# Performance work log

Measured on AMD Instinct MI355X. Metric: run time of the kernel, lower is better.

The kernel has to match this reference:

```python
import jax, jax.numpy as jnp
import numpy as np

N_NODES = 50000
N_EDGES = 600000
IN_FEATS = 128
H_FEATS = 128
NUM_CLASSES = 64


def setup_inputs() -> dict:
    key = jax.random.key(0)
    k = jax.random.split(key, 8)
    x = jax.random.normal(k[0], (N_NODES, IN_FEATS), dtype=jnp.float32)
    W1 = jax.random.normal(k[1], (IN_FEATS, H_FEATS), dtype=jnp.float32) * (1.0 / np.sqrt(IN_FEATS))
    b1 = jnp.zeros((H_FEATS,), dtype=jnp.float32)
    W2 = jax.random.normal(k[2], (H_FEATS, NUM_CLASSES), dtype=jnp.float32) * (1.0 / np.sqrt(H_FEATS))
    b2 = jnp.zeros((NUM_CLASSES,), dtype=jnp.float32)
    src = jax.random.randint(k[3], (N_EDGES,), 0, N_NODES, dtype=jnp.int64)
    dst = jax.random.randint(k[4], (N_EDGES,), 0, N_NODES, dtype=jnp.int64)
    return {"x": x, "W1": W1, "b1": b1, "W2": W2, "b2": b2, "src": src, "dst": dst}


def _graph_conv(h, W, b, src, dst, norm_src, norm_dst, n_nodes):
    # DGL GraphConv, norm='both': scale by 1/sqrt(out_deg(src)), sum over edges,
    # scale by 1/sqrt(in_deg(dst)), then linear transform.
    h = h * norm_src[:, None]                                   # [N, F]
    m = jax.ops.segment_sum(h[src], dst, num_segments=n_nodes)  # [N, F] scatter-add over edges
    m = m * norm_dst[:, None]
    return m @ W + b


def reference(x, W1, b1, W2, b2, src, dst):
    n = x.shape[0]
    ones = jnp.ones(src.shape[0], dtype=x.dtype)
    deg_out = jax.ops.segment_sum(ones, src, num_segments=n)
    deg_in = jax.ops.segment_sum(ones, dst, num_segments=n)
    norm_src = jax.lax.rsqrt(jnp.maximum(deg_out, 1.0))
    norm_dst = jax.lax.rsqrt(jnp.maximum(deg_in, 1.0))
    h = _graph_conv(x, W1, b1, src, dst, norm_src, norm_dst, n)
    h = jax.nn.relu(h)
    out = _graph_conv(h, W2, b2, src, dst, norm_src, norm_dst, n)
    return out
```

## Files before the change

### kernel.cpp

```cpp
#include <hip/hip_runtime.h>
#include <hip/hip_fp16.h>

#define NN 50000
#define NE 600000
#define KF 128
#define OC1 128
#define OC2 64

#define HBLK 64
#define HCH ((NE + HBLK - 1) / HBLK)
#define HP4 (NN / 4)
#define NSCB 49
#define NGB ((NN + 63) / 64)

typedef _Float16 half8 __attribute__((ext_vector_type(8)));
typedef float floatx4 __attribute__((ext_vector_type(4)));

__launch_bounds__(256)
__global__ void wt_hist_kernel(const float* __restrict__ W1, const float* __restrict__ W2,
                               __half* __restrict__ Wt1, __half* __restrict__ Wt2,
                               const int* __restrict__ src, const int* __restrict__ dst,
                               int* __restrict__ Hs, int* __restrict__ Hd) {
    __shared__ int bins[HP4];
    if (blockIdx.x < 96) {
        int i = blockIdx.x * 256 + threadIdx.x;
        if (i < KF * OC1) {
            int k = i >> 7, c = i & (OC1 - 1);
            Wt1[c * KF + k] = __float2half(W1[i]);
        } else {
            int j = i - KF * OC1;
            int k = j >> 6, c = j & (OC2 - 1);
            Wt2[c * KF + k] = __float2half(W2[j]);
        }
        return;
    }
    const int b = blockIdx.x - 96;
    const bool is_src = (b < HBLK);
    const int bb = is_src ? b : b - HBLK;
    const int* key = is_src ? src : dst;
    int* H = is_src ? Hs : Hd;
    const int e0 = bb * HCH;
    const int e1 = min(e0 + HCH, NE);

    for (int i = threadIdx.x; i < HP4; i += 256) bins[i] = 0;
    __syncthreads();
    for (int e = e0 + threadIdx.x; e < e1; e += 256) {
        int v = key[e];
        atomicAdd(&bins[v >> 2], 1 << ((v & 3) * 8));
    }
    __syncthreads();
    int* o = H + (size_t)bb * HP4;
    for (int i = threadIdx.x; i < HP4; i += 256) o[i] = bins[i];
}

__launch_bounds__(256)
__global__ void rednorm_kernel(const int* __restrict__ Hs, const int* __restrict__ Hd,
                               int* __restrict__ deg_i, float* __restrict__ nsrc,
                               float* __restrict__ ndst, int* __restrict__ bsum) {
    __shared__ int red[256];
    const int tid = threadIdx.x;
    const int p = blockIdx.x * 256 + tid;
    int so0 = 0, so1 = 0, so2 = 0, so3 = 0, si0 = 0, si1 = 0, si2 = 0, si3 = 0;
    if (p < HP4) {
#pragma unroll 4
        for (int b = 0; b < HBLK; b++) {
            int hs = Hs[(size_t)b * HP4 + p];
            int hd = Hd[(size_t)b * HP4 + p];
            so0 += hs & 255; so1 += (hs >> 8) & 255; so2 += (hs >> 16) & 255; so3 += (hs >> 24) & 255;
            si0 += hd & 255; si1 += (hd >> 8) & 255; si2 += (hd >> 16) & 255; si3 += (hd >> 24) & 255;
        }
        reinterpret_cast<int4*>(deg_i)[p] = make_int4(si0, si1, si2, si3);
        reinterpret_cast<float4*>(nsrc)[p] =
            make_float4(rsqrtf(fmaxf((float)so0, 1.f)), rsqrtf(fmaxf((float)so1, 1.f)),
                        rsqrtf(fmaxf((float)so2, 1.f)), rsqrtf(fmaxf((float)so3, 1.f)));
        reinterpret_cast<float4*>(ndst)[p] =
            make_float4(rsqrtf(fmaxf((float)si0, 1.f)), rsqrtf(fmaxf((float)si1, 1.f)),
                        rsqrtf(fmaxf((float)si2, 1.f)), rsqrtf(fmaxf((float)si3, 1.f)));
    }
    red[tid] = si0 + si1 + si2 + si3;
    __syncthreads();
    for (int off = 128; off > 0; off >>= 1) {
        if (tid < off) red[tid] += red[tid + off];
        __syncthreads();
    }
    if (tid == 0) bsum[blockIdx.x] = red[0];
}

__launch_bounds__(256)
__global__ void scan_bofs_gemm1_kernel(const int* __restrict__ deg, const int* __restrict__ bsum,
                                       const int* __restrict__ Hd, int* __restrict__ ptr,
                                       unsigned int* __restrict__ Bofs,
                                       const float* __restrict__ x, const __half* __restrict__ Wt1,
                                       const float* __restrict__ nsrc, __half* __restrict__ g) {
    extern __shared__ char smem[];
    if (blockIdx.x < NSCB) {
        int* s = (int*)smem;
        int* sboff = (int*)(smem + 1024);
        const int tid = threadIdx.x;
        if (tid < 64) {
            int v = (tid < (int)blockIdx.x) ? bsum[tid] : 0;
#pragma unroll
            for (int off = 32; off > 0; off >>= 1) v += __shfl_xor(v, off);
            if (tid == 0) *sboff = v;
        }
        const int q = blockIdx.x * 256 + tid;
        int4 d = make_int4(0, 0, 0, 0);
        if (q < HP4) d = reinterpret_cast<const int4*>(deg)[q];
        int t4 = d.x + d.y + d.z + d.w;
        s[tid] = t4;
        __syncthreads();
        for (int off = 1; off < 256; off <<= 1) {
            int t = (tid >= off) ? s[tid - off] : 0;
            __syncthreads();
            s[tid] += t;
            __syncthreads();
        }
        if (q < HP4) {
            int base = *sboff + s[tid] - t4;
            int4 pv;
            pv.x = base;
            pv.y = base + d.x;
            pv.z = pv.y + d.y;
            pv.w = pv.z + d.z;
            reinterpret_cast<int4*>(ptr)[q] = pv;
        }
        if (blockIdx.x == 0 && tid == 0) ptr[NN] = NE;
        return;
    }
    if (blockIdx.x < 2 * NSCB) {
        int p = (blockIdx.x - NSCB) * 256 + threadIdx.x;
        if (p >= HP4) return;
        int r0 = 0, r1 = 0, r2 = 0, r3 = 0;
#pragma unroll 4
        for (int b = 0; b < HBLK; b++) {
            Bofs[(size_t)b * HP4 + p] =
                (unsigned)(r0 | (r1 << 8) | (r2 << 16) | (r3 << 24));
            int h = Hd[(size_t)b * HP4 + p];
            r0 += h & 255; r1 += (h >> 8) & 255; r2 += (h >> 16) & 255; r3 += (h >> 24) & 255;
        }
        return;
    }
    constexpr int NT = OC1 / 16;
    constexpr int LDK = KF + 8;
    _Float16* Wsh = (_Float16*)smem;

    const int tid = threadIdx.x;
    const int wave = tid >> 6;
    const int lane = tid & 63;
    const int l16 = lane & 15;
    const int koff = (lane >> 4) * 8;
    const int row0 = (blockIdx.x - 2 * NSCB) * 64;
    const int arow = row0 + wave * 16 + l16;

    for (int i = tid; i < OC1 * (KF / 8); i += 256) {
        int r = i >> 4;
        int c8 = i & 15;
        *reinterpret_cast<uint4*>(&Wsh[r * LDK + c8 * 8]) =
            reinterpret_cast<const uint4*>(Wt1 + (size_t)r * KF)[c8];
    }

    half8 afr[4];
    if (arow < NN) {
        const float* ap = x + (size_t)arow * KF + koff;
#pragma unroll
        for (int kk = 0; kk < 4; kk++) {
            float4 v0 = *reinterpret_cast<const float4*>(ap + kk * 32);
            float4 v1 = *reinterpret_cast<const float4*>(ap + kk * 32 + 4);
            half8 h;
            h[0] = (_Float16)v0.x; h[1] = (_Float16)v0.y;
            h[2] = (_Float16)v0.z; h[3] = (_Float16)v0.w;
            h[4] = (_Float16)v1.x; h[5] = (_Float16)v1.y;
            h[6] = (_Float16)v1.z; h[7] = (_Float16)v1.w;
            afr[kk] = h;
        }
    } else {
#pragma unroll
        for (int kk = 0; kk < 4; kk++) afr[kk] = (half8)(_Float16)0;
    }

    __syncthreads();

    floatx4 acc[NT];
#pragma unroll
    for (int n = 0; n < NT; n++) acc[n] = (floatx4)(0.f);

#pragma unroll
    for (int n = 0; n < NT; n++) {
        const int brow = n * 16 + l16;
#pragma unroll
        for (int kk = 0; kk < 4; kk++) {
            half8 bfr = *reinterpret_cast<const half8*>(&Wsh[brow * LDK + kk * 32 + koff]);
            acc[n] = __builtin_amdgcn_mfma_f32_16x16x32_f16(afr[kk], bfr, acc[n], 0, 0, 0);
        }
    }

    const int crow = row0 + wave * 16 + (lane >> 4) * 4;
    float nsv[4];
#pragma unroll
    for (int j = 0; j < 4; j++) {
        int rr = crow + j;
        nsv[j] = (rr < NN) ? nsrc[rr] : 0.f;
    }
#pragma unroll
    for (int n = 0; n < NT; n++) {
#pragma unroll
        for (int j = 0; j < 4; j++) {
            int rr = crow + j;
            if (rr < NN)
                g[(size_t)rr * OC1 + n * 16 + l16] = __float2half(acc[n][j] * nsv[j]);
        }
    }
}

__launch_bounds__(256)
__global__ void fill_kernel(const int* __restrict__ src, const int* __restrict__ dst,
                            const unsigned int* __restrict__ Bofs,
                            const int* __restrict__ ptr, int* __restrict__ esrc) {
    __shared__ int cnt[HP4];
    const int b = blockIdx.x;
    const int e0 = b * HCH;
    const int e1 = min(e0 + HCH, NE);
    for (int i = threadIdx.x; i < HP4; i += 256) cnt[i] = 0;
    __syncthreads();
    const unsigned char* B = (const unsigned char*)(Bofs + (size_t)b * HP4);
    for (int e = e0 + threadIdx.x; e < e1; e += 256) {
        int v = dst[e];
        int sh = (v & 3) * 8;
        int old = atomicAdd(&cnt[v >> 2], 1 << sh);
        int idx = (old >> sh) & 255;
        esrc[ptr[v] + (int)B[v] + idx] = src[e];
    }
}

__launch_bounds__(256)
__global__ void gathergemm2_kernel(const __half* __restrict__ g, const int* __restrict__ ptr,
                                   const int* __restrict__ esrc, const float* __restrict__ ndst,
                                   const float* __restrict__ nsrc, const float* __restrict__ b1,
                                   const __half* __restrict__ Wt2, __half* __restrict__ g2) {
    constexpr int LDK = KF + 8;
    __shared__ _Float16 h1sh[64 * LDK];
    __shared__ _Float16 Wsh[OC2 * LDK];

    const int tid = threadIdx.x;
    const int node0 = blockIdx.x * 64;

    for (int i = tid; i < OC2 * (KF / 8); i += 256) {
        int r = i >> 4;
        int c8 = i & 15;
        *reinterpret_cast<uint4*>(&Wsh[r * LDK + c8 * 8]) =
            reinterpret_cast<const uint4*>(Wt2 + (size_t)r * KF)[c8];
    }

    const int qw = tid >> 4;
    const int l16g = tid & 15;
    const float4 bb0 = *reinterpret_cast<const float4*>(b1 + l16g * 8);
    const float4 bb1 = *reinterpret_cast<const float4*>(b1 + l16g * 8 + 4);
#pragma unroll 1
    for (int i = 0; i < 4; i++) {
        const int ln = qw + 16 * i;
        const int n = node0 + ln;
        if (n >= NN) continue;
        const int lo = ptr[n];
        const int hi = ptr[n + 1];
        const float nd = ndst[n];
        float4 a0 = make_float4(0.f, 0.f, 0.f, 0.f);
        float4 a1 = make_float4(0.f, 0.f, 0.f, 0.f);
        int e = lo;
        for (; e + 7 < hi; e += 8) {
            int s[8];
#pragma unroll
            for (int j = 0; j < 8; j++) s[j] = esrc[e + j];
            uint4 u[8];
#pragma unroll
            for (int j = 0; j < 8; j++)
                u[j] = *reinterpret_cast<const uint4*>(g + (size_t)s[j] * 128 + l16g * 8);
#pragma unroll
            for (int j = 0; j < 8; j++) {
                float2 f0 = __half22float2(*reinterpret_cast<__half2*>(&u[j].x));
                float2 f1 = __half22float2(*reinterpret_cast<__half2*>(&u[j].y));
                float2 f2 = __half22float2(*reinterpret_cast<__half2*>(&u[j].z));
                float2 f3 = __half22float2(*reinterpret_cast<__half2*>(&u[j].w));
                a0.x += f0.x; a0.y += f0.y; a0.z += f1.x; a0.w += f1.y;
                a1.x += f2.x; a1.y += f2.y; a1.z += f3.x; a1.w += f3.y;
            }
        }
        for (; e < hi; e++) {
            uint4 u = *reinterpret_cast<const uint4*>(g + (size_t)esrc[e] * 128 + l16g * 8);
            float2 f0 = __half22float2(*reinterpret_cast<__half2*>(&u.x));
            float2 f1 = __half22float2(*reinterpret_cast<__half2*>(&u.y));
            float2 f2 = __half22float2(*reinterpret_cast<__half2*>(&u.z));
            float2 f3 = __half22float2(*reinterpret_cast<__half2*>(&u.w));
            a0.x += f0.x; a0.y += f0.y; a0.z += f1.x; a0.w += f1.y;
            a1.x += f2.x; a1.y += f2.y; a1.z += f3.x; a1.w += f3.y;
        }
        const float ns = nsrc[n];
        float o0 = ns * fmaxf(fmaf(a0.x, nd, bb0.x), 0.f);
        float o1 = ns * fmaxf(fmaf(a0.y, nd, bb0.y), 0.f);
        float o2 = ns * fmaxf(fmaf(a0.z, nd, bb0.z), 0.f);
        float o3 = ns * fmaxf(fmaf(a0.w, nd, bb0.w), 0.f);
        float o4 = ns * fmaxf(fmaf(a1.x, nd, bb1.x), 0.f);
        float o5 = ns * fmaxf(fmaf(a1.y, nd, bb1.y), 0.f);
        float o6 = ns * fmaxf(fmaf(a1.z, nd, bb1.z), 0.f);
        float o7 = ns * fmaxf(fmaf(a1.w, nd, bb1.w), 0.f);
        __half2 h0 = __floats2half2_rn(o0, o1);
        __half2 h1v = __floats2half2_rn(o2, o3);
        __half2 h2 = __floats2half2_rn(o4, o5);
        __half2 h3 = __floats2half2_rn(o6, o7);
        uint4 pk;
        pk.x = *reinterpret_cast<unsigned int*>(&h0);
        pk.y = *reinterpret_cast<unsigned int*>(&h1v);
        pk.z = *reinterpret_cast<unsigned int*>(&h2);
        pk.w = *reinterpret_cast<unsigned int*>(&h3);
        *reinterpret_cast<uint4*>(&h1sh[ln * LDK + l16g * 8]) = pk;
    }
    __syncthreads();

    const int wave = tid >> 6;
    const int lane = tid & 63;
    const int l16 = lane & 15;
    const int koff = (lane >> 4) * 8;
    const int arow = wave * 16 + l16;

    half8 afr[4];
#pragma unroll
    for (int kk = 0; kk < 4; kk++)
        afr[kk] = *reinterpret_cast<const half8*>(&h1sh[arow * LDK + kk * 32 + koff]);

    floatx4 acc[4];
#pragma unroll
    for (int n = 0; n < 4; n++) acc[n] = (floatx4)(0.f);

#pragma unroll
    for (int n = 0; n < 4; n++) {
        const int brow = n * 16 + l16;
#pragma unroll
        for (int kk = 0; kk < 4; kk++) {
            half8 bfr = *reinterpret_cast<const half8*>(&Wsh[brow * LDK + kk * 32 + koff]);
            acc[n] = __builtin_amdgcn_mfma_f32_16x16x32_f16(afr[kk], bfr, acc[n], 0, 0, 0);
        }
    }

    const int crow = wave * 16 + (lane >> 4) * 4;
#pragma unroll
    for (int n = 0; n < 4; n++) {
#pragma unroll
        for (int j = 0; j < 4; j++) {
            int rr = node0 + crow + j;
            if (rr < NN)
                g2[(size_t)rr * OC2 + n * 16 + l16] = __float2half(acc[n][j]);
        }
    }
}

__launch_bounds__(256)
__global__ void gather64_kernel(const __half* __restrict__ g, const int* __restrict__ ptr,
                                const int* __restrict__ esrc, const float* __restrict__ ndst,
                                const float* __restrict__ bias, float* __restrict__ out) {
    const int node = blockIdx.x * 32 + (threadIdx.x >> 3);
    if (node >= NN) return;
    const int l8 = threadIdx.x & 7;
    const int cofs = l8 * 8;
    const int lo = ptr[node];
    const int hi = ptr[node + 1];
    const float nd = ndst[node];

    float4 ax[8], ay[8];
#pragma unroll
    for (int i = 0; i < 8; i++) {
        ax[i] = make_float4(0.f, 0.f, 0.f, 0.f);
        ay[i] = make_float4(0.f, 0.f, 0.f, 0.f);
    }

    int e = lo;
    for (; e + 7 < hi; e += 8) {
        int s[8];
#pragma unroll
        for (int i = 0; i < 8; i++) s[i] = esrc[e + i];
#pragma unroll
        for (int i = 0; i < 8; i++) {
            uint4 u = *reinterpret_cast<const uint4*>(g + (size_t)s[i] * 64 + cofs);
            float2 f0 = __half22float2(*reinterpret_cast<__half2*>(&u.x));
            float2 f1 = __half22float2(*reinterpret_cast<__half2*>(&u.y));
            float2 f2 = __half22float2(*reinterpret_cast<__half2*>(&u.z));
            float2 f3 = __half22float2(*reinterpret_cast<__half2*>(&u.w));
            ax[i].x += f0.x; ax[i].y += f0.y; ax[i].z += f1.x; ax[i].w += f1.y;
            ay[i].x += f2.x; ay[i].y += f2.y; ay[i].z += f3.x; ay[i].w += f3.y;
        }
    }
    for (; e < hi; e++) {
        uint4 u = *reinterpret_cast<const uint4*>(g + (size_t)esrc[e] * 64 + cofs);
        float2 f0 = __half22float2(*reinterpret_cast<__half2*>(&u.x));
        float2 f1 = __half22float2(*reinterpret_cast<__half2*>(&u.y));
        float2 f2 = __half22float2(*reinterpret_cast<__half2*>(&u.z));
        float2 f3 = __half22float2(*reinterpret_cast<__half2*>(&u.w));
        ax[0].x += f0.x; ax[0].y += f0.y; ax[0].z += f1.x; ax[0].w += f1.y;
        ay[0].x += f2.x; ay[0].y += f2.y; ay[0].z += f3.x; ay[0].w += f3.y;
    }
#pragma unroll
    for (int i = 1; i < 8; i++) {
        ax[0].x += ax[i].x; ax[0].y += ax[i].y; ax[0].z += ax[i].z; ax[0].w += ax[i].w;
        ay[0].x += ay[i].x; ay[0].y += ay[i].y; ay[0].z += ay[i].z; ay[0].w += ay[i].w;
    }

    float4 b0 = *reinterpret_cast<const float4*>(bias + cofs);
    float4 b1 = *reinterpret_cast<const float4*>(bias + cofs + 4);
    float4 o0, o1;
    o0.x = fmaf(ax[0].x, nd, b0.x); o0.y = fmaf(ax[0].y, nd, b0.y);
    o0.z = fmaf(ax[0].z, nd, b0.z); o0.w = fmaf(ax[0].w, nd, b0.w);
    o1.x = fmaf(ay[0].x, nd, b1.x); o1.y = fmaf(ay[0].y, nd, b1.y);
    o1.z = fmaf(ay[0].z, nd, b1.z); o1.w = fmaf(ay[0].w, nd, b1.w);
    float* op = out + (size_t)node * 64 + cofs;
    *reinterpret_cast<float4*>(op) = o0;
    *reinterpret_cast<float4*>(op + 4) = o1;
}

extern "C" void kernel_launch(void* const* d_in, const int* in_sizes, int n_in,
                              void* d_out, int out_size, void* d_ws, size_t ws_size,
                              hipStream_t stream) {
    const float* x  = (const float*)d_in[0];
    const float* W1 = (const float*)d_in[1];
    const float* b1 = (const float*)d_in[2];
    const float* W2 = (const float*)d_in[3];
    const float* b2 = (const float*)d_in[4];
    const int*   src = (const int*)d_in[5];
    const int*   dst = (const int*)d_in[6];
    float* out = (float*)d_out;

    __half* Wt1  = (__half*)d_ws;
    __half* Wt2  = Wt1 + KF * OC1;
    float*  nsrc = (float*)(Wt2 + KF * OC2);
    float*  ndst = nsrc + NN;
    __half* g    = (__half*)(ndst + NN);
    __half* g2   = g + (size_t)NN * KF;
    int* deg_i  = (int*)(g2 + (size_t)NN * OC2);
    int* ptr    = deg_i + NN;
    int* esrc   = ptr + NN + 4;
    int* bsum   = esrc + NE;
    int* Hs     = bsum + NSCB + 3;
    int* Hd     = Hs + (size_t)HBLK * HP4;
    unsigned int* Bofs = (unsigned int*)(Hd + (size_t)HBLK * HP4);

    wt_hist_kernel<<<96 + 2 * HBLK, 256, 0, stream>>>(W1, W2, Wt1, Wt2, src, dst, Hs, Hd);
    rednorm_kernel<<<NSCB, 256, 0, stream>>>(Hs, Hd, deg_i, nsrc, ndst, bsum);
    scan_bofs_gemm1_kernel<<<2 * NSCB + NGB, 256, OC1 * (KF + 8) * 2, stream>>>(
        deg_i, bsum, Hd, ptr, Bofs, x, Wt1, nsrc, g);
    fill_kernel<<<HBLK, 256, 0, stream>>>(src, dst, Bofs, ptr, esrc);
    gathergemm2_kernel<<<NGB, 256, 0, stream>>>(g, ptr, esrc, ndst, nsrc, b1, Wt2, g2);
    gather64_kernel<<<(NN + 31) / 32, 256, 0, stream>>>(g2, ptr, esrc, ndst, b2, out);
}
```

Baseline: 125.4 us.

## Load-balance gather in second layer by splitting block edges evenly across groups

In the second-layer gather+GEMM kernel, each block's contiguous edge range is now split evenly across 16 thread groups instead of assigning whole nodes to groups. Each group binary-searches its starting node and accumulates partial row sums, which it flushes with shared-memory float atomics into an fp32 staging buffer. A separate epilogue pass applies normalization, bias and ReLU, converts to fp16, and writes into the aliased tile for the MFMA stage. This targets imbalance from varying in-degrees, at the cost of more shared memory, extra zeroing, atomics and barriers.

After: 175.6 us. +40.0%, slower.

```diff
diff --git a/kernel.cpp b/kernel.cpp
--- a/kernel.cpp
+++ b/kernel.cpp
@@ -238,8 +238,10 @@
                                    const float* __restrict__ nsrc, const float* __restrict__ b1,
                                    const __half* __restrict__ Wt2, __half* __restrict__ g2) {
     constexpr int LDK = KF + 8;
-    __shared__ _Float16 h1sh[64 * LDK];
+    constexpr int LDA = KF + 4;
+    __shared__ float accf[64 * LDA];
     __shared__ _Float16 Wsh[OC2 * LDK];
+    __shared__ int sptr[65];
 
     const int tid = threadIdx.x;
     const int node0 = blockIdx.x * 64;
@@ -250,68 +252,106 @@
         *reinterpret_cast<uint4*>(&Wsh[r * LDK + c8 * 8]) =
             reinterpret_cast<const uint4*>(Wt2 + (size_t)r * KF)[c8];
     }
+    if (tid < 65) sptr[tid] = ptr[min(node0 + tid, NN)];
+    for (int i = tid; i < 64 * LDA; i += 256) accf[i] = 0.f;
+    __syncthreads();
 
     const int qw = tid >> 4;
     const int l16g = tid & 15;
-    const float4 bb0 = *reinterpret_cast<const float4*>(b1 + l16g * 8);
-    const float4 bb1 = *reinterpret_cast<const float4*>(b1 + l16g * 8 + 4);
-#pragma unroll 1
-    for (int i = 0; i < 4; i++) {
-        const int ln = qw + 16 * i;
-        const int n = node0 + ln;
-        if (n >= NN) continue;
-        const int lo = ptr[n];
-        const int hi = ptr[n + 1];
-        const float nd = ndst[n];
-        float4 a0 = make_float4(0.f, 0.f, 0.f, 0.f);
-        float4 a1 = make_float4(0.f, 0.f, 0.f, 0.f);
-        int e = lo;
-        for (; e + 7 < hi; e += 8) {
-            int s[8];
-#pragma unroll
-            for (int j = 0; j < 8; j++) s[j] = esrc[e + j];
-            uint4 u[8];
-#pragma unroll
-            for (int j = 0; j < 8; j++)
-                u[j] = *reinterpret_cast<const uint4*>(g + (size_t)s[j] * 128 + l16g * 8);
-#pragma unroll
-            for (int j = 0; j < 8; j++) {
-                float2 f0 = __half22float2(*reinterpret_cast<__half2*>(&u[j].x));
-                float2 f1 = __half22float2(*reinterpret_cast<__half2*>(&u[j].y));
-                float2 f2 = __half22float2(*reinterpret_cast<__half2*>(&u[j].z));
-                float2 f3 = __half22float2(*reinterpret_cast<__half2*>(&u[j].w));
-                a0.x += f0.x; a0.y += f0.y; a0.z += f1.x; a0.w += f1.y;
-                a1.x += f2.x; a1.y += f2.y; a1.z += f3.x; a1.w += f3.y;
+    {
+        const int ebase = sptr[0];
+        const int eend = sptr[64];
+        const int per = (eend - ebase + 15) >> 4;
+        int e = ebase + qw * per;
+        const int myE1 = min(e + per, eend);
+        if (e < myE1) {
+            int lo = 0, hi = 63;
+            while (lo < hi) {
+                int mid = (lo + hi + 1) >> 1;
+                if (sptr[mid] <= e) lo = mid; else hi = mid - 1;
             }
-        }
-        for (; e < hi; e++) {
-            uint4 u = *reinterpret_cast<const uint4*>(g + (size_t)esrc[e] * 128 + l16g * 8);
-            float2 f0 = __half22float2(*reinterpret_cast<__half2*>(&u.x));
-            float2 f1 = __half22float2(*reinterpret_cast<__half2*>(&u.y));
-            float2 f2 = __half22float2(*reinterpret_cast<__half2*>(&u.z));
-            float2 f3 = __half22float2(*reinterpret_cast<__half2*>(&u.w));
-            a0.x += f0.x; a0.y += f0.y; a0.z += f1.x; a0.w += f1.y;
-            a1.x += f2.x; a1.y += f2.y; a1.z += f3.x; a1.w += f3.y;
-        }
-        const float ns = nsrc[n];
-        float o0 = ns * fmaxf(fmaf(a0.x, nd, bb0.x), 0.f);
-        float o1 = ns * fmaxf(fmaf(a0.y, nd, bb0.y), 0.f);
-        float o2 = ns * fmaxf(fmaf(a0.z, nd, bb0.z), 0.f);
-        float o3 = ns * fmaxf(fmaf(a0.w, nd, bb0.w), 0.f);
-        float o4 = ns * fmaxf(fmaf(a1.x, nd, bb1.x), 0.f);
-        float o5 = ns * fmaxf(fmaf(a1.y, nd, bb1.y), 0.f);
-        float o6 = ns * fmaxf(fmaf(a1.z, nd, bb1.z), 0.f);
-        float o7 = ns * fmaxf(fmaf(a1.w, nd, bb1.w), 0.f);
+            int cur = lo;
+            while (e < myE1) {
+                while (sptr[cur + 1] <= e) cur++;
+                const int rend = min(myE1, sptr[cur + 1]);
+                float4 a0 = make_float4(0.f, 0.f, 0.f, 0.f);
+                float4 a1 = make_float4(0.f, 0.f, 0.f, 0.f);
+                for (; e + 7 < rend; e += 8) {
+                    int s[8];
+#pragma unroll
+                    for (int j = 0; j < 8; j++) s[j] = esrc[e + j];
+                    uint4 u[8];
+#pragma unroll
+                    for (int j = 0; j < 8; j++)
+                        u[j] = *reinterpret_cast<const uint4*>(g + (size_t)s[j] * 128 + l16g * 8);
+#pragma unroll
+                    for (int j = 0; j < 8; j++) {
+                        float2 f0 = __half22float2(*reinterpret_cast<__half2*>(&u[j].x));
+                        float2 f1 = __half22float2(*reinterpret_cast<__half2*>(&u[j].y));
+                        float2 f2 = __half22float2(*reinterpret_cast<__half2*>(&u[j].z));
+                        float2 f3 = __half22float2(*reinterpret_cast<__half2*>(&u[j].w));
+                        a0.x += f0.x; a0.y += f0.y; a0.z += f1.x; a0.w += f1.y;
+                        a1.x += f2.x; a1.y += f2.y; a1.z += f3.x; a1.w += f3.y;
+                    }
+                }
+                for (; e < rend; e++) {
+                    uint4 u = *reinterpret_cast<const uint4*>(g + (size_t)esrc[e] * 128 + l16g * 8);
+                    float2 f0 = __half22float2(*reinterpret_cast<__half2*>(&u.x));
+                    float2 f1 = __half22float2(*reinterpret_cast<__half2*>(&u.y));
+                    float2 f2 = __half22float2(*reinterpret_cast<__half2*>(&u.z));
+                    float2 f3 = __half22float2(*reinterpret_cast<__half2*>(&u.w));
+                    a0.x += f0.x; a0.y += f0.y; a0.z += f1.x; a0.w += f1.y;
+                    a1.x += f2.x; a1.y += f2.y; a1.z += f3.x; a1.w += f3.y;
+                }
+                float* ap = &accf[cur * LDA + l16g * 8];
+                atomicAdd(ap + 0, a0.x); atomicAdd(ap + 1, a0.y);
+                atomicAdd(ap + 2, a0.z); atomicAdd(ap + 3, a0.w);
+                atomicAdd(ap + 4, a1.x); atomicAdd(ap + 5, a1.y);
+                atomicAdd(ap + 6, a1.z); atomicAdd(ap + 7, a1.w);
+            }
+        }
+    }
+    __syncthreads();
+
+    _Float16* h1sh = (_Float16*)accf;
+    uint4 pk[4];
+#pragma unroll
+    for (int k = 0; k < 4; k++) {
+        const int i = tid + 256 * k;
+        const int r = i >> 4;
+        const int cg = i & 15;
+        const int n = node0 + r;
+        const float nd = (n < NN) ? ndst[n] : 0.f;
+        const float ns = (n < NN) ? nsrc[n] : 0.f;
+        const float* ap = &accf[r * LDA + cg * 8];
+        float4 v0 = *reinterpret_cast<const float4*>(ap);
+        float4 v1 = *reinterpret_cast<const float4*>(ap + 4);
+        float4 bb0 = *reinterpret_cast<const float4*>(b1 + cg * 8);
+        float4 bb1 = *reinterpret_cast<const float4*>(b1 + cg * 8 + 4);
+        float o0 = ns * fmaxf(fmaf(v0.x, nd, bb0.x), 0.f);
+        float o1 = ns * fmaxf(fmaf(v0.y, nd, bb0.y), 0.f);
+        float o2 = ns * fmaxf(fmaf(v0.z, nd, bb0.z), 0.f);
+        float o3 = ns * fmaxf(fmaf(v0.w, nd, bb0.w), 0.f);
+        float o4 = ns * fmaxf(fmaf(v1.x, nd, bb1.x), 0.f);
+        float o5 = ns * fmaxf(fmaf(v1.y, nd, bb1.y), 0.f);
+        float o6 = ns * fmaxf(fmaf(v1.z, nd, bb1.z), 0.f);
+        float o7 = ns * fmaxf(fmaf(v1.w, nd, bb1.w), 0.f);
         __half2 h0 = __floats2half2_rn(o0, o1);
         __half2 h1v = __floats2half2_rn(o2, o3);
         __half2 h2 = __floats2half2_rn(o4, o5);
         __half2 h3 = __floats2half2_rn(o6, o7);
-        uint4 pk;
-        pk.x = *reinterpret_cast<unsigned int*>(&h0);
-        pk.y = *reinterpret_cast<unsigned int*>(&h1v);
-        pk.z = *reinterpret_cast<unsigned int*>(&h2);
-        pk.w = *reinterpret_cast<unsigned int*>(&h3);
-        *reinterpret_cast<uint4*>(&h1sh[ln * LDK + l16g * 8]) = pk;
+        pk[k].x = *reinterpret_cast<unsigned int*>(&h0);
+        pk[k].y = *reinterpret_cast<unsigned int*>(&h1v);
+        pk[k].z = *reinterpret_cast<unsigned int*>(&h2);
+        pk[k].w = *reinterpret_cast<unsigned int*>(&h3);
+    }
+    __syncthreads();
+#pragma unroll
+    for (int k = 0; k < 4; k++) {
+        const int i = tid + 256 * k;
+        const int r = i >> 4;
+        const int cg = i & 15;
+        *reinterpret_cast<uint4*>(&h1sh[r * LDK + cg * 8]) = pk[k];
     }
     __syncthreads();
 
```
